# Optimization experiments

Measured on AMD Instinct MI355X. Metric: run time of the kernel, lower is better.

Reference implementation:

```python
import jax, jax.numpy as jnp
import numpy as np

D = 768          # embedding_dim
H = 8            # attention heads
DH = D // H
HID = 512        # hidden_dim
N_LAYERS = 3     # graph conv layers
N_ETYPES = 5
LN_EPS = 1e-5


def setup_inputs() -> dict:
    key = jax.random.key(0)
    ks = jax.random.split(key, 32)
    N, E = 4096, 131072
    s = lambda fan: 1.0 / np.sqrt(fan)
    inp = {
        'node_features': jax.random.normal(ks[0], (N, D), jnp.float32),
        'edge_indices': jax.random.randint(ks[1], (2, E), 0, N, jnp.int64),
        'edge_types': jax.random.randint(ks[2], (E,), 0, N_ETYPES, jnp.int64),
        'node_types': jax.random.randint(ks[3], (N,), 0, 3, jnp.int64),
        # embedding tables
        'statute_emb': jax.random.normal(ks[4], (1000, D), jnp.float32),
        'case_emb': jax.random.normal(ks[5], (5000, D), jnp.float32),
        'article_emb': jax.random.normal(ks[6], (2000, D), jnp.float32),
        # per-layer conv params (stacked over 3 layers)
        'conv_msg_W': jax.random.uniform(ks[7], (N_LAYERS, N_ETYPES, D, D), jnp.float32, -s(D), s(D)),
        'conv_msg_b': jax.random.uniform(ks[8], (N_LAYERS, N_ETYPES, D), jnp.float32, -s(D), s(D)),
        'conv_upd_W': jax.random.uniform(ks[9], (N_LAYERS, D, 2 * D), jnp.float32, -s(2 * D), s(2 * D)),
        'conv_upd_b': jax.random.uniform(ks[10], (N_LAYERS, D), jnp.float32, -s(2 * D), s(2 * D)),
        'conv_ln_g': jnp.ones((N_LAYERS, D), jnp.float32),
        'conv_ln_b': jnp.zeros((N_LAYERS, D), jnp.float32),
        # MultiheadAttention params
        'in_proj_W': jax.random.uniform(ks[11], (3 * D, D), jnp.float32, -s(D), s(D)),
        'in_proj_b': jnp.zeros((3 * D,), jnp.float32),
        'out_proj_W': jax.random.uniform(ks[12], (D, D), jnp.float32, -s(D), s(D)),
        'out_proj_b': jnp.zeros((D,), jnp.float32),
        # network analyzer MLP
        'an_W1': jax.random.uniform(ks[13], (HID, D), jnp.float32, -s(D), s(D)),
        'an_b1': jax.random.uniform(ks[14], (HID,), jnp.float32, -s(D), s(D)),
        'an_W2': jax.random.uniform(ks[15], (HID // 2, HID), jnp.float32, -s(HID), s(HID)),
        'an_b2': jax.random.uniform(ks[16], (HID // 2,), jnp.float32, -s(HID), s(HID)),
        'an_W3': jax.random.uniform(ks[17], (1, HID // 2), jnp.float32, -s(HID // 2), s(HID // 2)),
        'an_b3': jax.random.uniform(ks[18], (1,), jnp.float32, -s(HID // 2), s(HID // 2)),
    }
    return inp


def _layer_norm(h, g, b):
    mu = h.mean(-1, keepdims=True)
    var = ((h - mu) ** 2).mean(-1, keepdims=True)
    return g * (h - mu) / jnp.sqrt(var + LN_EPS) + b


def _conv_layer(x, msg_W, msg_b, upd_W, upd_b, ln_g, ln_b, src, tgt, etypes):
    # x: [N, D]; src/tgt: [E]; etypes: [E]
    src_feats = x[src]                               # gather [E, D]
    agg = jnp.zeros_like(x)
    for t in range(N_ETYPES):                        # small fixed loop over edge types
        mask = (etypes == t)[:, None]
        msgs = jnp.where(mask, src_feats @ msg_W[t].T + msg_b[t], 0.0)
        agg = agg + jax.ops.segment_sum(msgs, tgt, num_segments=x.shape[0])
    combined = jnp.concatenate([x, agg], axis=-1)    # [N, 2D]
    upd = jax.nn.relu(combined @ upd_W.T + upd_b)    # dropout is identity in eval
    return _layer_norm(x + upd, ln_g, ln_b)


def reference(node_features, edge_indices, edge_types, node_types,
              statute_emb, case_emb, article_emb,
              conv_msg_W, conv_msg_b, conv_upd_W, conv_upd_b, conv_ln_g, conv_ln_b,
              in_proj_W, in_proj_b, out_proj_W, out_proj_b,
              an_W1, an_b1, an_W2, an_b2, an_W3, an_b3):
    N = node_features.shape[0]
    idx = jnp.arange(N)
    # per-node-type embedding lookup (i % table_size), vectorized
    emb = jnp.where((node_types == 0)[:, None], statute_emb[idx % 1000],
          jnp.where((node_types == 1)[:, None], case_emb[idx % 5000],
                    article_emb[idx % 2000]))
    x = node_features + emb

    src, tgt = edge_indices[0], edge_indices[1]
    for l in range(N_LAYERS):
        x = _conv_layer(x, conv_msg_W[l], conv_msg_b[l], conv_upd_W[l], conv_upd_b[l],
                        conv_ln_g[l], conv_ln_b[l], src, tgt, edge_types)

    # self-attention over all nodes (batch of 1), torch MHA semantics, eval mode
    qkv = x @ in_proj_W.T + in_proj_b                # [N, 3D]
    q, k, v = jnp.split(qkv, 3, axis=-1)
    to_h = lambda t: t.reshape(N, H, DH).transpose(1, 0, 2)   # [H, N, DH]
    q, k, v = to_h(q), to_h(k), to_h(v)
    scores = jnp.einsum('hqd,hkd->hqk', q, k) / jnp.sqrt(jnp.float32(DH))
    attn = jax.nn.softmax(scores, axis=-1)           # [H, N, N]
    ctx = jnp.einsum('hqk,hkd->hqd', attn, v).transpose(1, 0, 2).reshape(N, D)
    graph_repr = ctx @ out_proj_W.T + out_proj_b     # [N, D]
    attn_weights = attn.mean(0)                      # averaged over heads [N, N]

    pooled = graph_repr.mean(axis=0)                 # [D]
    h = jax.nn.relu(pooled @ an_W1.T + an_b1)
    h = jax.nn.relu(h @ an_W2.T + an_b2)
    network_score = jax.nn.sigmoid(h @ an_W3.T + an_b3)

    return x, graph_repr, network_score, attn_weights
```

## Files before the change

### kernel.cpp

```cpp
#include <hip/hip_runtime.h>

typedef unsigned short u16;
typedef unsigned int u32;
typedef __attribute__((ext_vector_type(4))) float f32x4;
typedef __attribute__((ext_vector_type(8))) __bf16 bf16x8;
typedef __attribute__((ext_vector_type(4))) unsigned int u32x4;
typedef __attribute__((ext_vector_type(2))) unsigned int u32x2;

#define DEV static __device__ __forceinline__

#define NNODE 4096
#define DMODEL 768
#define NEDGE 131072

static constexpr size_t OFF_X     = 0;
static constexpr size_t OFF_X2    = 12582912;
static constexpr size_t OFF_AMSG  = 25165824;
static constexpr size_t OFF_AUPD  = 31457280;
static constexpr size_t OFF_WMSG  = 44040192;
static constexpr size_t OFF_WUPD  = 61734912;
static constexpr size_t OFF_WIP   = 68812800;
static constexpr size_t OFF_WOP   = 72351744;
static constexpr size_t OFF_Q     = 73531392;
static constexpr size_t OFF_K     = 79822848;
static constexpr size_t OFF_V     = 86114304;
static constexpr size_t OFF_CTX   = 92405760;
static constexpr size_t OFF_STATS = 98697216;
static constexpr size_t OFF_ML    = 98959360;
static constexpr size_t OFF_DEG   = 100007936;
static constexpr size_t OFF_OFFS  = 100024320;
static constexpr size_t OFF_CUR   = 100040960;
static constexpr size_t OFF_PACK  = 100057344;
static constexpr size_t OFF_PART  = 100581632;
static constexpr size_t OFF_POOL  = 101368064;
static constexpr size_t OFF_H1    = 101371136;
static constexpr size_t OFF_H2    = 101373184;
static constexpr size_t OFF_Y     = 101374208;
static constexpr size_t WS_TOTAL  = 132831488;

__device__ __attribute__((aligned(256))) unsigned char g_ws[WS_TOTAL];

DEV u16 f2bf(float f) {
  return __builtin_bit_cast(u16, (__bf16)f);
}
DEV float bf2f(u16 h) {
  union { unsigned u; float f; } v; v.u = ((unsigned)h) << 16;
  return v.f;
}
DEV void gl_lds16(const void* g, void* l) {
  __builtin_amdgcn_global_load_lds((const __attribute__((address_space(1))) void*)g,
                                   (__attribute__((address_space(3))) void*)l, 16, 0, 0);
}
DEV f32x4 mfma16(bf16x8 a, bf16x8 b, f32x4 c) {
  return __builtin_amdgcn_mfma_f32_16x16x32_bf16(a, b, c, 0, 0, 0);
}

__global__ void zero_kernel(int* p, int n) {
  int i = blockIdx.x * 256 + threadIdx.x;
  if (i < n) p[i] = 0;
}
__global__ void deg_kernel(const int* __restrict__ ei, int* __restrict__ deg) {
  int e = blockIdx.x * 256 + threadIdx.x;
  atomicAdd(&deg[ei[NEDGE + e]], 1);
}
__global__ void scan_kernel(const int* __restrict__ deg, int* __restrict__ offs, int* __restrict__ cur) {
  __shared__ int buf[1024];
  int t = threadIdx.x;
  int v0 = deg[t*4], v1 = deg[t*4+1], v2 = deg[t*4+2], v3 = deg[t*4+3];
  int s = v0 + v1 + v2 + v3;
  buf[t] = s;
  __syncthreads();
  for (int off = 1; off < 1024; off <<= 1) {
    int add = (t >= off) ? buf[t - off] : 0;
    __syncthreads();
    buf[t] += add;
    __syncthreads();
  }
  int run = buf[t] - s;
  offs[t*4] = run; cur[t*4] = run; run += v0;
  offs[t*4+1] = run; cur[t*4+1] = run; run += v1;
  offs[t*4+2] = run; cur[t*4+2] = run; run += v2;
  offs[t*4+3] = run; cur[t*4+3] = run; run += v3;
  if (t == 1023) offs[4096] = run;
}
__global__ void scatter_kernel(const int* __restrict__ ei, const int* __restrict__ ety,
                               int* __restrict__ cur, int* __restrict__ pack) {
  int e = blockIdx.x * 256 + threadIdx.x;
  int tg = ei[NEDGE + e];
  int pos = atomicAdd(&cur[tg], 1);
  pack[pos] = ei[e] | (ety[e] << 12);
}

__global__ void convert_bf_kernel(const float* __restrict__ W, u16* __restrict__ out, int total4) {
  for (int i = blockIdx.x * 256 + threadIdx.x; i < total4; i += gridDim.x * 256) {
    f32x4 w = *(const f32x4*)(W + (size_t)i * 4);
    u32x2 o;
    o.x = (u32)f2bf(w.x) | ((u32)f2bf(w.y) << 16);
    o.y = (u32)f2bf(w.z) | ((u32)f2bf(w.w) << 16);
    *(u32x2*)(out + (size_t)i * 4) = o;
  }
}

__global__ void embed_kernel(const float* __restrict__ nf, const int* __restrict__ nty,
                             const float* __restrict__ se, const float* __restrict__ ce,
                             const float* __restrict__ ae,
                             float* __restrict__ x, u16* __restrict__ Amsg, u16* __restrict__ Aupd) {
  int v = blockIdx.x, t = threadIdx.x;
  int typ = nty[v];
  const float* tab = (typ == 0) ? se + (size_t)(v % 1000) * 768
                   : (typ == 1) ? ce + (size_t)(v % 5000) * 768
                                : ae + (size_t)(v % 2000) * 768;
  #pragma unroll
  for (int i = 0; i < 3; ++i) {
    int c = t + i * 256;
    float f = nf[(size_t)v * 768 + c] + tab[c];
    x[(size_t)v * 768 + c] = f;
    u16 hi = f2bf(f);
    Amsg[(size_t)v * 768 + c] = hi;
    Aupd[(size_t)v * 1536 + c] = hi;
  }
}

template<int EPI>
__global__ void __launch_bounds__(256, 3)
gemm_bt(const u16* __restrict__ A, int lda,
        const u16* __restrict__ B0, int ldb, int K,
        const float* __restrict__ bias0,
        float* __restrict__ C0, int ldc,
        const float* __restrict__ resid,
        u16* __restrict__ oq, u16* __restrict__ okk, u16* __restrict__ ov,
        long zsB, int zsBias, long zsC)
{
  __shared__ alignas(16) u16 sA[8192];
  __shared__ alignas(16) u16 sB[8192];
  const int tid = threadIdx.x;
  const int lane = tid & 63, wid = tid >> 6;
  const int wr = wid >> 1, wc = wid & 1;
  const int li = lane & 15, g = lane >> 4;
  const int bm = blockIdx.y * 128, bn = blockIdx.x * 128;
  const int z = blockIdx.z;
  const u16* B = B0 + (size_t)z * zsB;
  const float* bias = bias0 + (size_t)z * zsBias;

  const int srow = tid >> 3;
  const int scol = ((tid & 7) ^ (srow & 7)) * 8;
  const u16* Ag = A + (size_t)(bm + srow) * lda + scol;
  const u16* Bg = B + (size_t)(bn + srow) * ldb + scol;
  char* sAw = (char*)sA + wid * 1024;
  char* sBw = (char*)sB + wid * 1024;

  f32x4 acc[4][4];
  const f32x4 vz = {0.f, 0.f, 0.f, 0.f};
  #pragma unroll
  for (int i = 0; i < 4; ++i)
    #pragma unroll
    for (int j = 0; j < 4; ++j) acc[i][j] = vz;

  for (int k0 = 0; k0 < K; k0 += 64) {
    __syncthreads();
    #pragma unroll
    for (int is = 0; is < 4; ++is) {
      gl_lds16(Ag + (size_t)is * 32 * lda + k0, sAw + is * 4096);
      gl_lds16(Bg + (size_t)is * 32 * ldb + k0, sBw + is * 4096);
    }
    __syncthreads();
    #pragma unroll
    for (int kc = 0; kc < 2; ++kc) {
      bf16x8 av[4], bv[4];
      #pragma unroll
      for (int mt = 0; mt < 4; ++mt) {
        int row = wr * 64 + mt * 16 + li;
        av[mt] = *(const bf16x8*)((const char*)sA + row * 128 + ((kc * 64 + g * 16) ^ ((row & 7) << 4)));
      }
      #pragma unroll
      for (int nt = 0; nt < 4; ++nt) {
        int row = wc * 64 + nt * 16 + li;
        bv[nt] = *(const bf16x8*)((const char*)sB + row * 128 + ((kc * 64 + g * 16) ^ ((row & 7) << 4)));
      }
      #pragma unroll
      for (int mt = 0; mt < 4; ++mt)
        #pragma unroll
        for (int nt = 0; nt < 4; ++nt)
          acc[mt][nt] = mfma16(av[mt], bv[nt], acc[mt][nt]);
    }
  }
  #pragma unroll
  for (int mt = 0; mt < 4; ++mt) {
    #pragma unroll
    for (int nt = 0; nt < 4; ++nt) {
      #pragma unroll
      for (int r = 0; r < 4; ++r) {
        int gr = bm + wr * 64 + mt * 16 + g * 4 + r;
        int gc = bn + wc * 64 + nt * 16 + li;
        float v = acc[mt][nt][r] + bias[gc];
        if (EPI == 0) {
          C0[(size_t)z * zsC + (size_t)gr * ldc + gc] = v;
        } else if (EPI == 1) {
          C0[(size_t)gr * ldc + gc] = fmaxf(v, 0.f) + resid[(size_t)gr * 768 + gc];
        } else if (EPI == 3) {
          oq[(size_t)z * zsC + (size_t)gr * ldc + gc] = f2bf(v);
        } else {
          int part = gc / 768;
          int j = gc - part * 768;
          int h = j / 96, d = j - h * 96;
          if (part == 0)      oq[((size_t)(h << 12) + gr) * 96 + d] = f2bf(v * 0.10206207261596575f);
          else if (part == 1) okk[((size_t)(h << 12) + gr) * 96 + d] = f2bf(v);
          else                ov[((size_t)h * 96 + d) * 4096 + gr] = f2bf(v);
        }
      }
    }
  }
}

__global__ void agg_kernel(const u16* __restrict__ Y, const int* __restrict__ offs,
                           const int* __restrict__ pack, u16* __restrict__ Aupd) {
  const int v = blockIdx.x, t = threadIdx.x;
  float a0 = 0.f, a1 = 0.f, a2 = 0.f, a3 = 0.f;
  const int beg = offs[v], end = offs[v + 1];
  const u32* Yw = (const u32*)Y;
  for (int i = beg; i < end; ++i) {
    int p = pack[i];
    u32x2 w = *(const u32x2*)(Yw + (size_t)p * 384 + t * 2);
    a0 += bf2f((u16)(w.x & 0xffffu));
    a1 += bf2f((u16)(w.x >> 16));
    a2 += bf2f((u16)(w.y & 0xffffu));
    a3 += bf2f((u16)(w.y >> 16));
  }
  u32x2 o;
  o.x = (u32)f2bf(a0) | ((u32)f2bf(a1) << 16);
  o.y = (u32)f2bf(a2) | ((u32)f2bf(a3) << 16);
  *(u32x2*)((u32*)(Aupd + (size_t)v * 1536 + 768) + t * 2) = o;
}

__global__ void ln_kernel(const float* __restrict__ xin, const float* __restrict__ gam,
                          const float* __restrict__ bet,
                          float* __restrict__ x, u16* __restrict__ Amsg, u16* __restrict__ Aupd,
                          float* __restrict__ xcopy) {
  __shared__ float red[256];
  int v = blockIdx.x, t = threadIdx.x;
  const float* r = xin + (size_t)v * 768;
  float v0 = r[t], v1 = r[t + 256], v2 = r[t + 512];
  red[t] = v0 + v1 + v2;
  __syncthreads();
  for (int off = 128; off > 0; off >>= 1) { if (t < off) red[t] += red[t + off]; __syncthreads(); }
  float mu = red[0] * (1.f / 768.f);
  __syncthreads();
  float d0 = v0 - mu, d1 = v1 - mu, d2 = v2 - mu;
  red[t] = d0 * d0 + d1 * d1 + d2 * d2;
  __syncthreads();
  for (int off = 128; off > 0; off >>= 1) { if (t < off) red[t] += red[t + off]; __syncthreads(); }
  float rstd = rsqrtf(red[0] * (1.f / 768.f) + 1e-5f);
  float dv[3] = {d0, d1, d2};
  #pragma unroll
  for (int i = 0; i < 3; ++i) {
    int c = t + i * 256;
    float y = gam[c] * dv[i] * rstd + bet[c];
    x[(size_t)v * 768 + c] = y;
    if (xcopy) xcopy[(size_t)v * 768 + c] = y;
    u16 hi = f2bf(y);
    Amsg[(size_t)v * 768 + c] = hi;
    Aupd[(size_t)v * 1536 + c] = hi;
  }
}

__global__ void __launch_bounds__(256, 3)
flash_kernel(const u16* __restrict__ Qb, const u16* __restrict__ Kb,
             const u16* __restrict__ Vtb, float* __restrict__ Op,
             float* __restrict__ Mp, float* __restrict__ Lp) {
  __shared__ alignas(16) u16 sK[6144];
  __shared__ alignas(16) u16 sV[6144];
  __shared__ alignas(16) u16 sP[4][2048];
  const int tid = threadIdx.x, lane = tid & 63, wid = tid >> 6;
  const int li = lane & 15, g = lane >> 4;
  const int qt = blockIdx.x, h = blockIdx.y, kcb = blockIdx.z;
  const int vrow = tid >> 3, vcol = (tid & 7) ^ (vrow & 7);

  const u16* Qg = Qb + ((size_t)(h << 12) + qt * 128 + wid * 32 + li) * 96 + g * 8;
  bf16x8 aq0[3], aq1[3];
  #pragma unroll
  for (int kc = 0; kc < 3; ++kc) {
    aq0[kc] = *(const bf16x8*)(Qg + kc * 32);
    aq1[kc] = *(const bf16x8*)(Qg + 1536 + kc * 32);
  }

  float m0 = -1e30f, l0 = 0.f, m1 = -1e30f, l1 = 0.f;
  const f32x4 vz = {0.f, 0.f, 0.f, 0.f};
  f32x4 o0[6], o1[6];
  #pragma unroll
  for (int dt = 0; dt < 6; ++dt) { o0[dt] = vz; o1[dt] = vz; }

  const char* Kg = (const char*)(Kb + (size_t)(h << 12) * 96);
  const char* Vg = (const char*)(Vtb + (size_t)h * 96 * 4096);
  char* sKb = (char*)sK; char* sVb = (char*)sV; char* sPb = (char*)sP[wid];

  for (int kt = kcb * 16; kt < kcb * 16 + 16; ++kt) {
    __syncthreads();
    #pragma unroll
    for (int j = 0; j < 3; ++j) {
      gl_lds16(Kg + ((size_t)(kt * 64 + lane) * 96 + j * 32 + wid * 8) * 2, sKb + j * 4096 + wid * 1024);
      gl_lds16(Vg + (size_t)(j * 32 + vrow) * 8192 + kt * 128 + vcol * 16, sVb + j * 4096 + wid * 1024);
    }
    __syncthreads();

    f32x4 s0[4], s1[4];
    __builtin_amdgcn_s_setprio(1);
    #pragma unroll
    for (int nt = 0; nt < 4; ++nt) {
      s0[nt] = vz; s1[nt] = vz;
      #pragma unroll
      for (int kc = 0; kc < 3; ++kc) {
        bf16x8 bk = *(const bf16x8*)(sKb + kc * 4096 + g * 1024 + (nt * 16 + li) * 16);
        s0[nt] = mfma16(bk, aq0[kc], s0[nt]);
        s1[nt] = mfma16(bk, aq1[kc], s1[nt]);
      }
    }
    __builtin_amdgcn_s_setprio(0);

    {
      float mx = fmaxf(fmaxf(fmaxf(s0[0][0], s0[0][1]), fmaxf(s0[0][2], s0[0][3])),
                       fmaxf(fmaxf(s0[1][0], s0[1][1]), fmaxf(s0[1][2], s0[1][3])));
      mx = fmaxf(mx, fmaxf(fmaxf(fmaxf(s0[2][0], s0[2][1]), fmaxf(s0[2][2], s0[2][3])),
                           fmaxf(fmaxf(s0[3][0], s0[3][1]), fmaxf(s0[3][2], s0[3][3]))));
      mx = fmaxf(mx, __shfl_xor(mx, 16));
      mx = fmaxf(mx, __shfl_xor(mx, 32));
      float mnew = fmaxf(m0, mx);
      float alpha = __expf(m0 - mnew);
      float rs = 0.f;
      #pragma unroll
      for (int nt = 0; nt < 4; ++nt)
        #pragma unroll
        for (int r = 0; r < 4; ++r) { float p = __expf(s0[nt][r] - mnew); s0[nt][r] = p; rs += p; }
      rs += __shfl_xor(rs, 16);
      rs += __shfl_xor(rs, 32);
      l0 = l0 * alpha + rs;
      m0 = mnew;
      #pragma unroll
      for (int dt = 0; dt < 6; ++dt) o0[dt] *= alpha;
      #pragma unroll
      for (int nt = 0; nt < 4; ++nt)
        #pragma unroll
        for (int r0 = 0; r0 < 4; r0 += 2) {
          u32 w = (u32)f2bf(s0[nt][r0]) | ((u32)f2bf(s0[nt][r0 + 1]) << 16);
          *(u32*)(sPb + li * 128 + (((nt * 16 + g * 4 + r0) * 2) ^ ((li & 7) << 4))) = w;
        }
    }
    {
      float mx = fmaxf(fmaxf(fmaxf(s1[0][0], s1[0][1]), fmaxf(s1[0][2], s1[0][3])),
                       fmaxf(fmaxf(s1[1][0], s1[1][1]), fmaxf(s1[1][2], s1[1][3])));
      mx = fmaxf(mx, fmaxf(fmaxf(fmaxf(s1[2][0], s1[2][1]), fmaxf(s1[2][2], s1[2][3])),
                           fmaxf(fmaxf(s1[3][0], s1[3][1]), fmaxf(s1[3][2], s1[3][3]))));
      mx = fmaxf(mx, __shfl_xor(mx, 16));
      mx = fmaxf(mx, __shfl_xor(mx, 32));
      float mnew = fmaxf(m1, mx);
      float alpha = __expf(m1 - mnew);
      float rs = 0.f;
      #pragma unroll
      for (int nt = 0; nt < 4; ++nt)
        #pragma unroll
        for (int r = 0; r < 4; ++r) { float p = __expf(s1[nt][r] - mnew); s1[nt][r] = p; rs += p; }
      rs += __shfl_xor(rs, 16);
      rs += __shfl_xor(rs, 32);
      l1 = l1 * alpha + rs;
      m1 = mnew;
      #pragma unroll
      for (int dt = 0; dt < 6; ++dt) o1[dt] *= alpha;
      #pragma unroll
      for (int nt = 0; nt < 4; ++nt)
        #pragma unroll
        for (int r0 = 0; r0 < 4; r0 += 2) {
          u32 w = (u32)f2bf(s1[nt][r0]) | ((u32)f2bf(s1[nt][r0 + 1]) << 16);
          *(u32*)(sPb + (16 + li) * 128 + (((nt * 16 + g * 4 + r0) * 2) ^ ((li & 7) << 4))) = w;
        }
    }

    __builtin_amdgcn_s_setprio(1);
    #pragma unroll
    for (int kc2 = 0; kc2 < 2; ++kc2) {
      bf16x8 pa0 = *(const bf16x8*)(sPb + li * 128 + ((kc2 * 64 + g * 16) ^ ((li & 7) << 4)));
      bf16x8 pa1 = *(const bf16x8*)(sPb + (16 + li) * 128 + ((kc2 * 64 + g * 16) ^ ((li & 7) << 4)));
      #pragma unroll
      for (int dt = 0; dt < 6; ++dt) {
        int d = dt * 16 + li;
        bf16x8 bvv = *(const bf16x8*)(sVb + d * 128 + ((kc2 * 64 + g * 16) ^ ((d & 7) << 4)));
        o0[dt] = mfma16(pa0, bvv, o0[dt]);
        o1[dt] = mfma16(pa1, bvv, o1[dt]);
      }
    }
    __builtin_amdgcn_s_setprio(0);
  }
  int bq = qt * 128 + wid * 32;
  size_t cb = (size_t)(((kcb * 8 + h) << 12));
  #pragma unroll
  for (int dt = 0; dt < 6; ++dt)
    #pragma unroll
    for (int r = 0; r < 4; ++r) {
      int d = dt * 16 + li;
      Op[(cb + bq + g * 4 + r) * 96 + d] = o0[dt][r];
      Op[(cb + bq + 16 + g * 4 + r) * 96 + d] = o1[dt][r];
    }
  if (g == 0) {
    Mp[cb + bq + li] = m0;      Lp[cb + bq + li] = l0;
    Mp[cb + bq + 16 + li] = m1; Lp[cb + bq + 16 + li] = l1;
  }
}

__global__ void merge_kernel(const float* __restrict__ Op, const float* __restrict__ Mp,
                             const float* __restrict__ Lp,
                             u16* __restrict__ ctxb, float* __restrict__ stats) {
  int row = blockIdx.x, t = threadIdx.x;
  #pragma unroll
  for (int i = 0; i < 3; ++i) {
    int idx = t + i * 256;
    int h = idx / 96, d = idx - h * 96;
    int base = (h << 12) + row;
    float m0 = Mp[base], m1 = Mp[32768 + base], m2 = Mp[65536 + base], m3 = Mp[98304 + base];
    float M = fmaxf(fmaxf(m0, m1), fmaxf(m2, m3));
    float w0 = __expf(m0 - M), w1 = __expf(m1 - M), w2 = __expf(m2 - M), w3 = __expf(m3 - M);
    float L = w0 * Lp[base] + w1 * Lp[32768 + base] + w2 * Lp[65536 + base] + w3 * Lp[98304 + base];
    float o = w0 * Op[(size_t)base * 96 + d]
            + w1 * Op[(size_t)(32768 + base) * 96 + d]
            + w2 * Op[(size_t)(65536 + base) * 96 + d]
            + w3 * Op[(size_t)(98304 + base) * 96 + d];
    float invl = 1.f / L;
    ctxb[(size_t)row * 768 + idx] = f2bf(o * invl);
    if (d == 0) {
      stats[base] = M;
      stats[32768 + base] = invl;
    }
  }
}

__global__ void __launch_bounds__(256, 3)
mean_kernel(const u16* __restrict__ Qb, const u16* __restrict__ Kb,
            const float* __restrict__ stats, float* __restrict__ out) {
  __shared__ alignas(16) u16 sQ[12288];
  __shared__ alignas(16) u16 sK2[6144];
  const int tid = threadIdx.x, lane = tid & 63, wid = tid >> 6;
  const int li = lane & 15, g = lane >> 4;
  const int q0 = blockIdx.x * 128, k0 = blockIdx.y * 64;
  const f32x4 vz = {0.f, 0.f, 0.f, 0.f};
  f32x4 macc0[4], macc1[4];
  #pragma unroll
  for (int nt = 0; nt < 4; ++nt) { macc0[nt] = vz; macc1[nt] = vz; }
  char* sQb = (char*)sQ; char* sKb = (char*)sK2;
  const int rq = (wid & 1) * 64 + lane;
  const int ccb = wid >> 1;

  for (int h = 0; h < 8; ++h) {
    __syncthreads();
    #pragma unroll
    for (int i = 0; i < 6; ++i) {
      int cc = i * 2 + ccb, kc = cc >> 2, gg = cc & 3;
      gl_lds16((const char*)Qb + ((size_t)(h << 12) + q0 + rq) * 192 + kc * 64 + gg * 16,
               sQb + kc * 8192 + gg * 2048 + (wid & 1) * 1024);
    }
    #pragma unroll
    for (int i = 0; i < 3; ++i) {
      int c = i * 4 + wid, kc = c >> 2, gg = c & 3;
      gl_lds16((const char*)Kb + ((size_t)(h << 12) + k0 + lane) * 192 + kc * 64 + gg * 16,
               sKb + kc * 4096 + gg * 1024);
    }
    __syncthreads();

    bf16x8 a20[3], a21[3];
    #pragma unroll
    for (int kc = 0; kc < 3; ++kc) {
      a20[kc] = *(const bf16x8*)(sQb + kc * 8192 + g * 2048 + (wid * 32 + li) * 16);
      a21[kc] = *(const bf16x8*)(sQb + kc * 8192 + g * 2048 + (wid * 32 + 16 + li) * 16);
    }
    f32x4 s0[4], s1[4];
    __builtin_amdgcn_s_setprio(1);
    #pragma unroll
    for (int nt = 0; nt < 4; ++nt) {
      s0[nt] = vz; s1[nt] = vz;
      #pragma unroll
      for (int kc = 0; kc < 3; ++kc) {
        bf16x8 bk = *(const bf16x8*)(sKb + kc * 4096 + g * 1024 + (nt * 16 + li) * 16);
        s0[nt] = mfma16(a20[kc], bk, s0[nt]);
        s1[nt] = mfma16(a21[kc], bk, s1[nt]);
      }
    }
    __builtin_amdgcn_s_setprio(0);
    #pragma unroll
    for (int r = 0; r < 4; ++r) {
      int row0 = q0 + wid * 32 + g * 4 + r;
      float mm0 = stats[(h << 12) + row0];
      float si0 = 0.125f * stats[32768 + (h << 12) + row0];
      int row1 = row0 + 16;
      float mm1 = stats[(h << 12) + row1];
      float si1 = 0.125f * stats[32768 + (h << 12) + row1];
      #pragma unroll
      for (int nt = 0; nt < 4; ++nt) {
        macc0[nt][r] += __expf(s0[nt][r] - mm0) * si0;
        macc1[nt][r] += __expf(s1[nt][r] - mm1) * si1;
      }
    }
  }
  #pragma unroll
  for (int nt = 0; nt < 4; ++nt)
    #pragma unroll
    for (int r = 0; r < 4; ++r) {
      out[(size_t)(q0 + wid * 32 + g * 4 + r) * 4096 + k0 + nt * 16 + li] = macc0[nt][r];
      out[(size_t)(q0 + wid * 32 + 16 + g * 4 + r) * 4096 + k0 + nt * 16 + li] = macc1[nt][r];
    }
}

__global__ void colsum_kernel(const float* __restrict__ gr, float* __restrict__ part) {
  int b = blockIdx.x, t = threadIdx.x;
  float s0 = 0.f, s1 = 0.f, s2 = 0.f;
  for (int rr = 0; rr < 16; ++rr) {
    const float* row = gr + (size_t)(b * 16 + rr) * 768;
    s0 += row[t]; s1 += row[t + 256]; s2 += row[t + 512];
  }
  part[b * 768 + t] = s0; part[b * 768 + t + 256] = s1; part[b * 768 + t + 512] = s2;
}
__global__ void pool_kernel(const float* __restrict__ part, float* __restrict__ pool) {
  int t = blockIdx.x * 256 + threadIdx.x;
  float s = 0.f;
  for (int b = 0; b < 256; ++b) s += part[b * 768 + t];
  pool[t] = s * (1.f / 4096.f);
}
template<int KDIM>
__global__ void mlp_fc_kernel(const float* __restrict__ in, const float* __restrict__ Wm,
                              const float* __restrict__ bb, float* __restrict__ outv) {
  int o = blockIdx.x * 4 + (threadIdx.x >> 6);
  int lane = threadIdx.x & 63;
  const float* w = Wm + (size_t)o * KDIM;
  float s = 0.f;
  #pragma unroll
  for (int k = lane; k < KDIM; k += 64) s += w[k] * in[k];
  s += __shfl_xor(s, 1);  s += __shfl_xor(s, 2);  s += __shfl_xor(s, 4);
  s += __shfl_xor(s, 8);  s += __shfl_xor(s, 16); s += __shfl_xor(s, 32);
  if (lane == 0) outv[o] = fmaxf(s + bb[o], 0.f);
}
__global__ void mlp3_kernel(const float* __restrict__ h2,
                            const float* __restrict__ W3, const float* __restrict__ b3,
                            float* __restrict__ out) {
  __shared__ float red[256];
  int t = threadIdx.x;
  red[t] = W3[t] * h2[t];
  __syncthreads();
  for (int off = 128; off > 0; off >>= 1) { if (t < off) red[t] += red[t + off]; __syncthreads(); }
  if (t == 0) out[0] = 1.f / (1.f + __expf(-(red[0] + b3[0])));
}

extern "C" void kernel_launch(void* const* d_in, const int* in_sizes, int n_in,
                              void* d_out, int out_size, void* d_ws, size_t ws_size,
                              hipStream_t stream) {
  const float* nf   = (const float*)d_in[0];
  const int*   ei   = (const int*)d_in[1];
  const int*   ety  = (const int*)d_in[2];
  const int*   nty  = (const int*)d_in[3];
  const float* se   = (const float*)d_in[4];
  const float* ce   = (const float*)d_in[5];
  const float* ae   = (const float*)d_in[6];
  const float* msgW = (const float*)d_in[7];
  const float* msgb = (const float*)d_in[8];
  const float* updW = (const float*)d_in[9];
  const float* updb = (const float*)d_in[10];
  const float* lng  = (const float*)d_in[11];
  const float* lnb  = (const float*)d_in[12];
  const float* ipW  = (const float*)d_in[13];
  const float* ipb  = (const float*)d_in[14];
  const float* opW  = (const float*)d_in[15];
  const float* opb  = (const float*)d_in[16];
  const float* aW1  = (const float*)d_in[17];
  const float* ab1  = (const float*)d_in[18];
  const float* aW2  = (const float*)d_in[19];
  const float* ab2  = (const float*)d_in[20];
  const float* aW3  = (const float*)d_in[21];
  const float* ab3  = (const float*)d_in[22];

  void* wsp = nullptr;
  hipGetSymbolAddress(&wsp, HIP_SYMBOL(g_ws));
  unsigned char* W = (unsigned char*)wsp;

  float* x     = (float*)(W + OFF_X);
  float* x2    = (float*)(W + OFF_X2);
  u16* Amsg    = (u16*)(W + OFF_AMSG);
  u16* Aupd    = (u16*)(W + OFF_AUPD);
  u16* Wmsg    = (u16*)(W + OFF_WMSG);
  u16* Wupd    = (u16*)(W + OFF_WUPD);
  u16* Wip     = (u16*)(W + OFF_WIP);
  u16* Wop     = (u16*)(W + OFF_WOP);
  u16* Qb      = (u16*)(W + OFF_Q);
  u16* Kb      = (u16*)(W + OFF_K);
  u16* Vtb     = (u16*)(W + OFF_V);
  u16* Ctxb    = (u16*)(W + OFF_CTX);
  float* stats = (float*)(W + OFF_STATS);
  float* Mp    = (float*)(W + OFF_ML);
  float* Lp    = Mp + 131072;
  int* deg     = (int*)(W + OFF_DEG);
  int* offs    = (int*)(W + OFF_OFFS);
  int* cur     = (int*)(W + OFF_CUR);
  int* pack    = (int*)(W + OFF_PACK);
  float* part  = (float*)(W + OFF_PART);
  float* pool  = (float*)(W + OFF_POOL);
  float* h1b   = (float*)(W + OFF_H1);
  float* h2b   = (float*)(W + OFF_H2);
  u16*   Yb    = (u16*)(W + OFF_Y);

  float* out_x    = (float*)d_out;
  float* out_gr   = out_x + (size_t)NNODE * DMODEL;
  float* out_sc   = out_gr + (size_t)NNODE * DMODEL;
  float* out_attn = out_sc + 1;
  float* Op       = out_attn;

  zero_kernel<<<16, 256, 0, stream>>>(deg, NNODE);
  deg_kernel<<<NEDGE / 256, 256, 0, stream>>>(ei, deg);
  scan_kernel<<<1, 1024, 0, stream>>>(deg, offs, cur);
  scatter_kernel<<<NEDGE / 256, 256, 0, stream>>>(ei, ety, cur, pack);

  convert_bf_kernel<<<2048, 256, 0, stream>>>(msgW, Wmsg, 3 * 5 * 768 * 768 / 4);
  convert_bf_kernel<<<1024, 256, 0, stream>>>(updW, Wupd, 3 * 768 * 1536 / 4);
  convert_bf_kernel<<<1024, 256, 0, stream>>>(ipW, Wip, 2304 * 768 / 4);
  convert_bf_kernel<<<512, 256, 0, stream>>>(opW, Wop, 768 * 768 / 4);

  embed_kernel<<<NNODE, 256, 0, stream>>>(nf, nty, se, ce, ae, x, Amsg, Aupd);

  for (int l = 0; l < 3; ++l) {
    gemm_bt<3><<<dim3(6, 32, 5), 256, 0, stream>>>(Amsg, 768,
        Wmsg + (size_t)l * 5 * 768 * 768, 768, 768,
        msgb + (size_t)l * 5 * 768, nullptr, 768, nullptr, Yb, nullptr, nullptr,
        (long)768 * 768, 768, (long)NNODE * DMODEL);
    agg_kernel<<<NNODE, 192, 0, stream>>>(Yb, offs, pack, Aupd);
    gemm_bt<1><<<dim3(6, 32, 1), 256, 0, stream>>>(Aupd, 1536,
        Wupd + (size_t)l * 768 * 1536, 1536, 1536,
        updb + (size_t)l * 768, x2, 768, x, nullptr, nullptr, nullptr, 0, 0, 0);
    ln_kernel<<<NNODE, 256, 0, stream>>>(x2, lng + (size_t)l * 768, lnb + (size_t)l * 768,
        x, Amsg, Aupd, (l == 2) ? out_x : nullptr);
  }

  gemm_bt<2><<<dim3(18, 32, 1), 256, 0, stream>>>(Amsg, 768, Wip, 768, 768,
      ipb, nullptr, 0, nullptr, Qb, Kb, Vtb, 0, 0, 0);
  flash_kernel<<<dim3(32, 8, 4), 256, 0, stream>>>(Qb, Kb, Vtb, Op, Mp, Lp);
  merge_kernel<<<NNODE, 256, 0, stream>>>(Op, Mp, Lp, Ctxb, stats);
  mean_kernel<<<dim3(32, 64), 256, 0, stream>>>(Qb, Kb, stats, out_attn);
  gemm_bt<0><<<dim3(6, 32, 1), 256, 0, stream>>>(Ctxb, 768, Wop, 768, 768,
      opb, out_gr, 768, nullptr, nullptr, nullptr, nullptr, 0, 0, 0);

  colsum_kernel<<<256, 256, 0, stream>>>(out_gr, part);
  pool_kernel<<<3, 256, 0, stream>>>(part, pool);
  mlp_fc_kernel<768><<<128, 256, 0, stream>>>(pool, aW1, ab1, h1b);
  mlp_fc_kernel<512><<<64, 256, 0, stream>>>(h1b, aW2, ab2, h2b);
  mlp3_kernel<<<1, 256, 0, stream>>>(h2b, aW3, ab3, out_sc);
}
```

Before: 640.2 us.

## Enlarge flash-attention query tile per wave and drop duplicate Amsg buffer

The flash attention kernel now gives each wave 64 query rows (four 16-row fragments) instead of 32, so each block covers 256 queries. Every K/V tile loaded into shared memory is therefore reused across twice as many MFMAs, and the grid is halved. The cost is much higher register pressure, so launch bounds drop to 2 blocks per CU, and the P buffer in shared memory doubles. Separately, the bf16 copy Amsg is removed and the GEMMs read the first half of Aupd with stride 1536, which saves one redundant store per element in the embed and layernorm kernels.

```diff
diff --git a/kernel.cpp b/kernel.cpp
--- a/kernel.cpp
+++ b/kernel.cpp
@@ -15,7 +15,6 @@
 
 static constexpr size_t OFF_X     = 0;
 static constexpr size_t OFF_X2    = 12582912;
-static constexpr size_t OFF_AMSG  = 25165824;
 static constexpr size_t OFF_AUPD  = 31457280;
 static constexpr size_t OFF_WMSG  = 44040192;
 static constexpr size_t OFF_WUPD  = 61734912;
@@ -104,7 +103,7 @@
 __global__ void embed_kernel(const float* __restrict__ nf, const int* __restrict__ nty,
                              const float* __restrict__ se, const float* __restrict__ ce,
                              const float* __restrict__ ae,
-                             float* __restrict__ x, u16* __restrict__ Amsg, u16* __restrict__ Aupd) {
+                             float* __restrict__ x, u16* __restrict__ Aupd) {
   int v = blockIdx.x, t = threadIdx.x;
   int typ = nty[v];
   const float* tab = (typ == 0) ? se + (size_t)(v % 1000) * 768
@@ -115,9 +114,7 @@
     int c = t + i * 256;
     float f = nf[(size_t)v * 768 + c] + tab[c];
     x[(size_t)v * 768 + c] = f;
-    u16 hi = f2bf(f);
-    Amsg[(size_t)v * 768 + c] = hi;
-    Aupd[(size_t)v * 1536 + c] = hi;
+    Aupd[(size_t)v * 1536 + c] = f2bf(f);
   }
 }
 
@@ -234,7 +231,7 @@
 
 __global__ void ln_kernel(const float* __restrict__ xin, const float* __restrict__ gam,
                           const float* __restrict__ bet,
-                          float* __restrict__ x, u16* __restrict__ Amsg, u16* __restrict__ Aupd,
+                          float* __restrict__ x, u16* __restrict__ Aupd,
                           float* __restrict__ xcopy) {
   __shared__ float red[256];
   int v = blockIdx.x, t = threadIdx.x;
@@ -257,37 +254,39 @@
     float y = gam[c] * dv[i] * rstd + bet[c];
     x[(size_t)v * 768 + c] = y;
     if (xcopy) xcopy[(size_t)v * 768 + c] = y;
-    u16 hi = f2bf(y);
-    Amsg[(size_t)v * 768 + c] = hi;
-    Aupd[(size_t)v * 1536 + c] = hi;
-  }
-}
-
-__global__ void __launch_bounds__(256, 3)
+    Aupd[(size_t)v * 1536 + c] = f2bf(y);
+  }
+}
+
+__global__ void __launch_bounds__(256, 2)
 flash_kernel(const u16* __restrict__ Qb, const u16* __restrict__ Kb,
              const u16* __restrict__ Vtb, float* __restrict__ Op,
              float* __restrict__ Mp, float* __restrict__ Lp) {
   __shared__ alignas(16) u16 sK[6144];
   __shared__ alignas(16) u16 sV[6144];
-  __shared__ alignas(16) u16 sP[4][2048];
+  __shared__ alignas(16) u16 sP[4][4096];
   const int tid = threadIdx.x, lane = tid & 63, wid = tid >> 6;
   const int li = lane & 15, g = lane >> 4;
   const int qt = blockIdx.x, h = blockIdx.y, kcb = blockIdx.z;
   const int vrow = tid >> 3, vcol = (tid & 7) ^ (vrow & 7);
 
-  const u16* Qg = Qb + ((size_t)(h << 12) + qt * 128 + wid * 32 + li) * 96 + g * 8;
-  bf16x8 aq0[3], aq1[3];
-  #pragma unroll
-  for (int kc = 0; kc < 3; ++kc) {
-    aq0[kc] = *(const bf16x8*)(Qg + kc * 32);
-    aq1[kc] = *(const bf16x8*)(Qg + 1536 + kc * 32);
-  }
-
-  float m0 = -1e30f, l0 = 0.f, m1 = -1e30f, l1 = 0.f;
+  const u16* Qg = Qb + ((size_t)(h << 12) + qt * 256 + wid * 64 + li) * 96 + g * 8;
+  bf16x8 aq[4][3];
+  #pragma unroll
+  for (int qf = 0; qf < 4; ++qf)
+    #pragma unroll
+    for (int kc = 0; kc < 3; ++kc)
+      aq[qf][kc] = *(const bf16x8*)(Qg + qf * 1536 + kc * 32);
+
+  float m[4], l[4];
+  #pragma unroll
+  for (int qf = 0; qf < 4; ++qf) { m[qf] = -1e30f; l[qf] = 0.f; }
   const f32x4 vz = {0.f, 0.f, 0.f, 0.f};
-  f32x4 o0[6], o1[6];
-  #pragma unroll
-  for (int dt = 0; dt < 6; ++dt) { o0[dt] = vz; o1[dt] = vz; }
+  f32x4 o[4][6];
+  #pragma unroll
+  for (int qf = 0; qf < 4; ++qf)
+    #pragma unroll
+    for (int dt = 0; dt < 6; ++dt) o[qf][dt] = vz;
 
   const char* Kg = (const char*)(Kb + (size_t)(h << 12) * 96);
   const char* Vg = (const char*)(Vtb + (size_t)h * 96 * 4096);
@@ -302,105 +301,85 @@
     }
     __syncthreads();
 
-    f32x4 s0[4], s1[4];
+    f32x4 s[4][4];
     __builtin_amdgcn_s_setprio(1);
     #pragma unroll
     for (int nt = 0; nt < 4; ++nt) {
-      s0[nt] = vz; s1[nt] = vz;
+      #pragma unroll
+      for (int qf = 0; qf < 4; ++qf) s[qf][nt] = vz;
       #pragma unroll
       for (int kc = 0; kc < 3; ++kc) {
         bf16x8 bk = *(const bf16x8*)(sKb + kc * 4096 + g * 1024 + (nt * 16 + li) * 16);
-        s0[nt] = mfma16(bk, aq0[kc], s0[nt]);
-        s1[nt] = mfma16(bk, aq1[kc], s1[nt]);
+        #pragma unroll
+        for (int qf = 0; qf < 4; ++qf)
+          s[qf][nt] = mfma16(bk, aq[qf][kc], s[qf][nt]);
       }
     }
     __builtin_amdgcn_s_setprio(0);
 
-    {
-      float mx = fmaxf(fmaxf(fmaxf(s0[0][0], s0[0][1]), fmaxf(s0[0][2], s0[0][3])),
-                       fmaxf(fmaxf(s0[1][0], s0[1][1]), fmaxf(s0[1][2], s0[1][3])));
-      mx = fmaxf(mx, fmaxf(fmaxf(fmaxf(s0[2][0], s0[2][1]), fmaxf(s0[2][2], s0[2][3])),
-                           fmaxf(fmaxf(s0[3][0], s0[3][1]), fmaxf(s0[3][2], s0[3][3]))));
+    #pragma unroll
+    for (int qf = 0; qf < 4; ++qf) {
+      float mx = fmaxf(fmaxf(fmaxf(s[qf][0][0], s[qf][0][1]), fmaxf(s[qf][0][2], s[qf][0][3])),
+                       fmaxf(fmaxf(s[qf][1][0], s[qf][1][1]), fmaxf(s[qf][1][2], s[qf][1][3])));
+      mx = fmaxf(mx, fmaxf(fmaxf(fmaxf(s[qf][2][0], s[qf][2][1]), fmaxf(s[qf][2][2], s[qf][2][3])),
+                           fmaxf(fmaxf(s[qf][3][0], s[qf][3][1]), fmaxf(s[qf][3][2], s[qf][3][3]))));
       mx = fmaxf(mx, __shfl_xor(mx, 16));
       mx = fmaxf(mx, __shfl_xor(mx, 32));
-      float mnew = fmaxf(m0, mx);
-      float alpha = __expf(m0 - mnew);
+      float mnew = fmaxf(m[qf], mx);
+      float alpha = __expf(m[qf] - mnew);
       float rs = 0.f;
       #pragma unroll
       for (int nt = 0; nt < 4; ++nt)
         #pragma unroll
-        for (int r = 0; r < 4; ++r) { float p = __expf(s0[nt][r] - mnew); s0[nt][r] = p; rs += p; }
+        for (int r = 0; r < 4; ++r) { float p = __expf(s[qf][nt][r] - mnew); s[qf][nt][r] = p; rs += p; }
       rs += __shfl_xor(rs, 16);
       rs += __shfl_xor(rs, 32);
-      l0 = l0 * alpha + rs;
-      m0 = mnew;
-      #pragma unroll
-      for (int dt = 0; dt < 6; ++dt) o0[dt] *= alpha;
-      #pragma unroll
-      for (int nt = 0; nt < 4; ++nt)
-        #pragma unroll
-        for (int r0 = 0; r0 < 4; r0 += 2) {
-          u32 w = (u32)f2bf(s0[nt][r0]) | ((u32)f2bf(s0[nt][r0 + 1]) << 16);
-          *(u32*)(sPb + li * 128 + (((nt * 16 + g * 4 + r0) * 2) ^ ((li & 7) << 4))) = w;
-        }
-    }
-    {
-      float mx = fmaxf(fmaxf(fmaxf(s1[0][0], s1[0][1]), fmaxf(s1[0][2], s1[0][3])),
-                       fmaxf(fmaxf(s1[1][0], s1[1][1]), fmaxf(s1[1][2], s1[1][3])));
-      mx = fmaxf(mx, fmaxf(fmaxf(fmaxf(s1[2][0], s1[2][1]), fmaxf(s1[2][2], s1[2][3])),
-                           fmaxf(fmaxf(s1[3][0], s1[3][1]), fmaxf(s1[3][2], s1[3][3]))));
-      mx = fmaxf(mx, __shfl_xor(mx, 16));
-      mx = fmaxf(mx, __shfl_xor(mx, 32));
-      float mnew = fmaxf(m1, mx);
-      float alpha = __expf(m1 - mnew);
-      float rs = 0.f;
-      #pragma unroll
-      for (int nt = 0; nt < 4; ++nt)
-        #pragma unroll
-        for (int r = 0; r < 4; ++r) { float p = __expf(s1[nt][r] - mnew); s1[nt][r] = p; rs += p; }
-      rs += __shfl_xor(rs, 16);
-      rs += __shfl_xor(rs, 32);
-      l1 = l1 * alpha + rs;
-      m1 = mnew;
-      #pragma unroll
-      for (int dt = 0; dt < 6; ++dt) o1[dt] *= alpha;
-      #pragma unroll
-      for (int nt = 0; nt < 4; ++nt)
-        #pragma unroll
-        for (int r0 = 0; r0 < 4; r0 += 2) {
-          u32 w = (u32)f2bf(s1[nt][r0]) | ((u32)f2bf(s1[nt][r0 + 1]) << 16);
-          *(u32*)(sPb + (16 + li) * 128 + (((nt * 16 + g * 4 + r0) * 2) ^ ((li & 7) << 4))) = w;
-        }
+      l[qf] = l[qf] * alpha + rs;
+      m[qf] = mnew;
+      #pragma unroll
+      for (int dt = 0; dt < 6; ++dt) o[qf][dt] *= alpha;
+      #pragma unroll
+      for (int nt = 0; nt < 4; ++nt) {
+        u32x2 w;
+        w.x = (u32)f2bf(s[qf][nt][0]) | ((u32)f2bf(s[qf][nt][1]) << 16);
+        w.y = (u32)f2bf(s[qf][nt][2]) | ((u32)f2bf(s[qf][nt][3]) << 16);
+        *(u32x2*)(sPb + (qf * 16 + li) * 128 + (((nt * 16 + g * 4) * 2) ^ ((li & 7) << 4))) = w;
+      }
     }
 
     __builtin_amdgcn_s_setprio(1);
     #pragma unroll
     for (int kc2 = 0; kc2 < 2; ++kc2) {
-      bf16x8 pa0 = *(const bf16x8*)(sPb + li * 128 + ((kc2 * 64 + g * 16) ^ ((li & 7) << 4)));
-      bf16x8 pa1 = *(const bf16x8*)(sPb + (16 + li) * 128 + ((kc2 * 64 + g * 16) ^ ((li & 7) << 4)));
+      bf16x8 pa[4];
+      #pragma unroll
+      for (int qf = 0; qf < 4; ++qf)
+        pa[qf] = *(const bf16x8*)(sPb + (qf * 16 + li) * 128 + ((kc2 * 64 + g * 16) ^ ((li & 7) << 4)));
       #pragma unroll
       for (int dt = 0; dt < 6; ++dt) {
         int d = dt * 16 + li;
         bf16x8 bvv = *(const bf16x8*)(sVb + d * 128 + ((kc2 * 64 + g * 16) ^ ((d & 7) << 4)));
-        o0[dt] = mfma16(pa0, bvv, o0[dt]);
-        o1[dt] = mfma16(pa1, bvv, o1[dt]);
+        #pragma unroll
+        for (int qf = 0; qf < 4; ++qf)
+          o[qf][dt] = mfma16(pa[qf], bvv, o[qf][dt]);
       }
     }
     __builtin_amdgcn_s_setprio(0);
   }
-  int bq = qt * 128 + wid * 32;
+  int bq = qt * 256 + wid * 64;
   size_t cb = (size_t)(((kcb * 8 + h) << 12));
   #pragma unroll
-  for (int dt = 0; dt < 6; ++dt)
-    #pragma unroll
-    for (int r = 0; r < 4; ++r) {
-      int d = dt * 16 + li;
-      Op[(cb + bq + g * 4 + r) * 96 + d] = o0[dt][r];
-      Op[(cb + bq + 16 + g * 4 + r) * 96 + d] = o1[dt][r];
-    }
-  if (g == 0) {
-    Mp[cb + bq + li] = m0;      Lp[cb + bq + li] = l0;
-    Mp[cb + bq + 16 + li] = m1; Lp[cb + bq + 16 + li] = l1;
+  for (int qf = 0; qf < 4; ++qf) {
+    #pragma unroll
+    for (int dt = 0; dt < 6; ++dt)
+      #pragma unroll
+      for (int r = 0; r < 4; ++r) {
+        int d = dt * 16 + li;
+        Op[(cb + bq + qf * 16 + g * 4 + r) * 96 + d] = o[qf][dt][r];
+      }
+    if (g == 0) {
+      Mp[cb + bq + qf * 16 + li] = m[qf];
+      Lp[cb + bq + qf * 16 + li] = l[qf];
+    }
   }
 }
 
@@ -577,7 +556,6 @@
 
   float* x     = (float*)(W + OFF_X);
   float* x2    = (float*)(W + OFF_X2);
-  u16* Amsg    = (u16*)(W + OFF_AMSG);
   u16* Aupd    = (u16*)(W + OFF_AUPD);
   u16* Wmsg    = (u16*)(W + OFF_WMSG);
   u16* Wupd    = (u16*)(W + OFF_WUPD);
@@ -616,10 +594,10 @@
   convert_bf_kernel<<<1024, 256, 0, stream>>>(ipW, Wip, 2304 * 768 / 4);
   convert_bf_kernel<<<512, 256, 0, stream>>>(opW, Wop, 768 * 768 / 4);
 
-  embed_kernel<<<NNODE, 256, 0, stream>>>(nf, nty, se, ce, ae, x, Amsg, Aupd);
+  embed_kernel<<<NNODE, 256, 0, stream>>>(nf, nty, se, ce, ae, x, Aupd);
 
   for (int l = 0; l < 3; ++l) {
-    gemm_bt<3><<<dim3(6, 32, 5), 256, 0, stream>>>(Amsg, 768,
+    gemm_bt<3><<<dim3(6, 32, 5), 256, 0, stream>>>(Aupd, 1536,
         Wmsg + (size_t)l * 5 * 768 * 768, 768, 768,
         msgb + (size_t)l * 5 * 768, nullptr, 768, nullptr, Yb, nullptr, nullptr,
         (long)768 * 768, 768, (long)NNODE * DMODEL);
@@ -628,12 +606,12 @@
         Wupd + (size_t)l * 768 * 1536, 1536, 1536,
         updb + (size_t)l * 768, x2, 768, x, nullptr, nullptr, nullptr, 0, 0, 0);
     ln_kernel<<<NNODE, 256, 0, stream>>>(x2, lng + (size_t)l * 768, lnb + (size_t)l * 768,
-        x, Amsg, Aupd, (l == 2) ? out_x : nullptr);
-  }
-
-  gemm_bt<2><<<dim3(18, 32, 1), 256, 0, stream>>>(Amsg, 768, Wip, 768, 768,
+        x, Aupd, (l == 2) ? out_x : nullptr);
+  }
+
+  gemm_bt<2><<<dim3(18, 32, 1), 256, 0, stream>>>(Aupd, 1536, Wip, 768, 768,
       ipb, nullptr, 0, nullptr, Qb, Kb, Vtb, 0, 0, 0);
-  flash_kernel<<<dim3(32, 8, 4), 256, 0, stream>>>(Qb, Kb, Vtb, Op, Mp, Lp);
+  flash_kernel<<<dim3(16, 8, 4), 256, 0, stream>>>(Qb, Kb, Vtb, Op, Mp, Lp);
   merge_kernel<<<NNODE, 256, 0, stream>>>(Op, Mp, Lp, Ctxb, stats);
   mean_kernel<<<dim3(32, 64), 256, 0, stream>>>(Qb, Kb, stats, out_attn);
   gemm_bt<0><<<dim3(6, 32, 1), 256, 0, stream>>>(Ctxb, 768, Wop, 768, 768,
```

Measured after the change: 653.8 us. 1.02x slower.
